# Kernel tuning notes

Measured on AMD Instinct MI355X. Metric: run time of the kernel, lower is better.

## Reference

```python
import jax, jax.numpy as jnp
import numpy as np

HID = 512      # out_channels / HR2O hidden_dim
CIN = 2048     # conv1 input channels (Cf + Cx)
DEPTH = 3
EPS = 1e-5     # GroupNorm eps


def conv2d(x, w, pad):
    return jax.lax.conv_general_dilated(
        x, w, window_strides=(1, 1), padding=[(pad, pad), (pad, pad)],
        dimension_numbers=('NCHW', 'OIHW', 'NCHW'))


def hr2o(x, wq, wk, wv, wm, gamma, beta):
    # x: [N, C, H, W]
    q = conv2d(x, wq, 1)
    k = conv2d(x, wk, 1)
    v = conv2d(x, wv, 1)
    # (query.unsqueeze(1) * key.unsqueeze(0)).sum(2) / sqrt(C) -> [N, N, H, W]
    att = jnp.einsum('qchw,kchw->qkhw', q, k) / jnp.sqrt(jnp.float32(HID))
    att = jax.nn.softmax(att, axis=1)  # softmax over key dim
    # (att.unsqueeze(2) * value).sum(1) -> [N, C, H, W]
    vf = jnp.einsum('qkhw,kchw->qchw', att, v)
    # GroupNorm(1, C): normalize over (C, H, W), per-channel affine
    mu = jnp.mean(vf, axis=(1, 2, 3), keepdims=True)
    var = jnp.var(vf, axis=(1, 2, 3), keepdims=True)
    vf = (vf - mu) * jax.lax.rsqrt(var + EPS)
    vf = vf * gamma[None, :, None, None] + beta[None, :, None, None]
    vf = jax.nn.relu(vf)
    vf = conv2d(vf, wm, 1)
    # Dropout(0.2) is identity in eval mode
    return x + vf


def setup_inputs() -> dict:
    key = jax.random.key(0)
    ks = jax.random.split(key, 12)
    N, B = 32, 8
    Cx, Cf, H, W = 1024, 1024, 16, 16
    s = 0.02
    return {
        'x': jax.random.normal(ks[0], (N, Cx, 4, 7, 7), jnp.float32),
        'feat': jax.random.normal(ks[1], (B, Cf, 1, H, W), jnp.float32),
        'rois': jax.random.randint(ks[2], (N, 5), 0, B, jnp.int32),
        'w1': jax.random.normal(ks[3], (HID, CIN, 1, 1), jnp.float32) * s,
        'w2': jax.random.normal(ks[4], (HID, HID, 3, 3), jnp.float32) * s,
        'wq': jax.random.normal(ks[5], (DEPTH, HID, HID, 3, 3), jnp.float32) * s,
        'wk': jax.random.normal(ks[6], (DEPTH, HID, HID, 3, 3), jnp.float32) * s,
        'wv': jax.random.normal(ks[7], (DEPTH, HID, HID, 3, 3), jnp.float32) * s,
        'wm': jax.random.normal(ks[8], (DEPTH, HID, HID, 3, 3), jnp.float32) * s,
        'gamma': jnp.ones((DEPTH, HID), jnp.float32),
        'beta': jnp.zeros((DEPTH, HID), jnp.float32),
    }


def reference(x, feat, rois, w1, w2, wq, wk, wv, wm, gamma, beta):
    n, cx = x.shape[0], x.shape[1]
    # AdaptiveMaxPool3d(1) -> [N, Cx, 1, 1, 1]
    xp = jnp.max(x, axis=(2, 3, 4), keepdims=True)
    h, w = feat.shape[-2], feat.shape[-1]
    roi_inds = rois[:, 0].astype(jnp.int32)
    roi_gfeat = feat[roi_inds]                              # [N, Cf, 1, H, W]
    x_tile = jnp.broadcast_to(xp, (n, cx, 1, h, w))         # repeat(1,1,1,h,w)
    nf = jnp.concatenate([roi_gfeat, x_tile], axis=1)[:, :, 0]  # squeeze(2)
    nf = jax.nn.relu(conv2d(nf, w1, 0))                     # 1x1 conv
    nf = jax.nn.relu(conv2d(nf, w2, 0))                     # 3x3 conv, no pad
    for i in range(DEPTH):
        nf = hr2o(nf, wq[i], wk[i], wv[i], wm[i], gamma[i], beta[i])
    nf = jnp.mean(nf, axis=(2, 3), keepdims=True)[:, :, None]  # gap -> [N,C,1,1,1]
    return jnp.concatenate([xp, nf], axis=1)                # [N, Cx+HID, 1, 1, 1]
```

## Files before the change

kernel.cpp:

```cpp
#include <hip/hip_runtime.h>


typedef __attribute__((ext_vector_type(8))) short bhalf8;
typedef __attribute__((ext_vector_type(4))) float floatx4;

#define ACT_N 131072
#define W3SZ  2359296

__device__ inline float b2f(unsigned short u) {
  union { unsigned int i; float f; } x; x.i = ((unsigned int)u) << 16; return x.f;
}
__device__ inline unsigned short f2b(float f) {
  union { float f; unsigned int i; } x; x.f = f;
  return (unsigned short)((x.i + 0x7FFFu + ((x.i >> 16) & 1u)) >> 16);
}
__device__ inline void gload_lds16(const unsigned short* g, bhalf8* l) {
  __builtin_amdgcn_global_load_lds(
      (const __attribute__((address_space(1))) unsigned int*)(const void*)g,
      (__attribute__((address_space(3))) unsigned int*)(void*)l, 16, 0, 0);
}
template <int N> __device__ inline void waitvm() {
  asm volatile("s_waitcnt vmcnt(%0)" :: "i"(N) : "memory");
}
__device__ inline void phase_barrier_pre() {
  __builtin_amdgcn_sched_barrier(0);
  __builtin_amdgcn_s_barrier();
  __builtin_amdgcn_sched_barrier(0);
}
__device__ inline void phase_barrier_post() {
  __builtin_amdgcn_sched_barrier(0);
  __builtin_amdgcn_s_barrier();
  __builtin_amdgcn_sched_barrier(0);
}

__global__ void pool_max_kernel(const float* __restrict__ x, float* __restrict__ xp,
                                float* __restrict__ out) {
  int tid = threadIdx.x;
  int wid = blockIdx.x * 4 + (tid >> 6);
  int lane = tid & 63;
  int n = wid >> 10, c = wid & 1023;
  const float* p = x + (size_t)wid * 196;
  float v = -3.4e38f;
  v = fmaxf(v, p[lane]);
  v = fmaxf(v, p[lane + 64]);
  v = fmaxf(v, p[lane + 128]);
  if (lane < 4) v = fmaxf(v, p[lane + 192]);
#pragma unroll
  for (int off = 32; off >= 1; off >>= 1) v = fmaxf(v, __shfl_xor(v, off));
  if (lane == 0) { xp[wid] = v; out[(size_t)n * 1536 + c] = v; }
}

__global__ void bias1_kernel(const float* __restrict__ w1, const float* __restrict__ xp,
                             float* __restrict__ bias1) {
  int tid = threadIdx.x;
  int wid = blockIdx.x * 4 + (tid >> 6);
  int lane = tid & 63;
  int n = wid >> 9, o = wid & 511;
  const float* wr = w1 + (size_t)o * 2048 + 1024;
  const float* xr = xp + (size_t)n * 1024;
  float s = 0.f;
#pragma unroll
  for (int r = 0; r < 16; r++) { int c = lane + r * 64; s += wr[c] * xr[c]; }
#pragma unroll
  for (int off = 32; off >= 1; off >>= 1) s += __shfl_xor(s, off);
  if (lane == 0) bias1[wid] = s;
}

__global__ __launch_bounds__(256) void wprep3_kernel(
    const float* __restrict__ w2, const float* __restrict__ wq,
    const float* __restrict__ wk, const float* __restrict__ wv,
    const float* __restrict__ wm, unsigned short* __restrict__ Wg2) {
  int ks = blockIdx.x, ot = blockIdx.y, tid = blockIdx.z;
  int t = threadIdx.x;
  const float* src;
  if (tid == 0) src = w2;
  else {
    int d = (tid - 1) >> 2, r = (tid - 1) & 3;
    src = (r == 0 ? wq : r == 1 ? wk : r == 2 ? wv : wm) + (size_t)d * W3SZ;
  }
  __shared__ unsigned short S[64 * 288];
  const float* sb = src + (size_t)ot * 64 * 4608 + (size_t)ks * 288;
  for (int j = 0; j < 72; j++) {
    int flat = j * 256 + t;
    int o = flat / 288, ci = flat % 288;
    S[flat] = f2b(sb[(size_t)o * 4608 + ci]);
  }
  __syncthreads();
  unsigned short* dst = Wg2 + (((size_t)(tid * 8 + ot) * 16 + ks) * 2304) * 8;
#pragma unroll
  for (int s = 0; s < 9; s++) {
    int u = t + s * 256;
    int g = u / 768, rem = u % 768;
    int rl = rem >> 6, o = rem & 63;
    int dh = rl >> 2, kg = rl & 3;
    int t9src = dh * 3 + g;
    bhalf8 v;
#pragma unroll
    for (int j = 0; j < 8; j++) v[j] = (short)S[o * 288 + (kg * 8 + j) * 9 + t9src];
    *(bhalf8*)(dst + (size_t)u * 8) = v;
  }
}

__global__ void w1prep_kernel(const float* __restrict__ w1, unsigned short* __restrict__ W1g) {
  int ks = blockIdx.x, ot = blockIdx.y, t = threadIdx.x;
  int kg = t >> 6, o = t & 63;
  const float* s = w1 + (size_t)(ot * 64 + o) * 2048 + ks * 32 + kg * 8;
  bhalf8 v;
#pragma unroll
  for (int j = 0; j < 8; j++) v[j] = (short)f2b(s[j]);
  *(bhalf8*)(W1g + (((size_t)ot * 32 + ks) * 256 + t) * 8) = v;
}

__global__ __launch_bounds__(256) void ftprep_kernel(
    const float* __restrict__ feat, unsigned short* __restrict__ featT) {
  int img = blockIdx.z, c0 = blockIdx.y * 64, p0 = blockIdx.x * 64;
  int t = threadIdx.x;
  int a = t >> 6, b = t & 63;
  __shared__ float S[64][65];
#pragma unroll
  for (int j = 0; j < 16; j++) {
    int r = a * 16 + j;
    S[r][b] = feat[((size_t)img * 1024 + c0 + r) * 256 + p0 + b];
  }
  __syncthreads();
#pragma unroll
  for (int j = 0; j < 16; j++) {
    int pl = a * 16 + j;
    featT[((size_t)img * 256 + p0 + pl) * 1024 + c0 + b] = f2b(S[b][pl]);
  }
}

template <int TAPS, int KTOT, int WAVES, int NREP, int PSPLIT,
          bool RELU, bool ADD, bool BIAS, bool VALID>
__global__ __launch_bounds__(WAVES * 64) void conv_mfma_kernel(
    const unsigned short* __restrict__ Xg, const int* __restrict__ rois,
    const unsigned short* __restrict__ Wg, const float* __restrict__ bias,
    unsigned short* __restrict__ Out) {
  constexpr int THREADS = WAVES * 64;
  constexpr int NK = KTOT / 32;
  static_assert(PSPLIT * WAVES * NREP * 16 == 256, "p coverage");

  int n = blockIdx.y;
  int ot = blockIdx.x / PSPLIT;
  int pq = blockIdx.x % PSPLIT;
  int t = threadIdx.x;
  int wv = t >> 6, l = t & 63, l15 = l & 15, l4 = l >> 4;
  int pbase = (pq * WAVES + wv) * (NREP * 16);
  const unsigned short* xb =
      Xg + (rois ? (size_t)rois[n * 5] * 256 * KTOT : (size_t)n * 256 * KTOT);
  floatx4 acc[4][NREP] = {};

  if constexpr (TAPS == 9) {
    constexpr int LW = 768 / THREADS;
    constexpr int LX = 1024 / THREADS;
    static_assert(768 % THREADS == 0 && 1024 % THREADS == 0, "stage div");
    __shared__ bhalf8 Xs[2][1024];
    __shared__ bhalf8 Wl[3][768];

    auto stageX = [&](int xbuf, int ks) {
#pragma unroll
      for (int i = 0; i < LX; i++) {
        int base = i * THREADS + wv * 64;
        int u = base + l;
        int p = u & 255, kg = u >> 8;
        gload_lds16(xb + (size_t)p * KTOT + ks * 32 + kg * 8, &Xs[xbuf][base]);
      }
    };
    auto stageW = [&](int wbuf, int ks, int g) {
      const unsigned short* wb =
          Wg + (((size_t)ot * NK + ks) * 2304 + g * 768) * 8;
#pragma unroll
      for (int i = 0; i < LW; i++) {
        int base = i * THREADS + wv * 64;
        gload_lds16(wb + (size_t)(base + l) * 8, &Wl[wbuf][base]);
      }
    };
    auto computeG = [&](const bhalf8* X, const bhalf8* W, int g) {
      bhalf8 BW[NREP + 2];
#pragma unroll
      for (int w10 = 0; w10 < NREP + 2; w10++) {
        int row = (pbase + w10 * 16 + l15 + g) & 255;
        BW[w10] = X[l4 * 256 + row];
      }
      bhalf8 A[3][4];
#pragma unroll
      for (int dh = 0; dh < 3; dh++)
#pragma unroll
        for (int of = 0; of < 4; of++)
          A[dh][of] = W[(dh * 4 + l4) * 64 + of * 16 + l15];
      __builtin_amdgcn_s_setprio(1);
#pragma unroll
      for (int dh = 0; dh < 3; dh++)
#pragma unroll
        for (int of = 0; of < 4; of++)
#pragma unroll
          for (int pf = 0; pf < NREP; pf++)
            acc[of][pf] = __builtin_amdgcn_mfma_f32_16x16x32_bf16(
                A[dh][of], BW[pf + dh], acc[of][pf], 0, 0, 0);
      __builtin_amdgcn_s_setprio(0);
    };

    stageW(0, 0, 0); stageX(0, 0);
    stageW(1, 0, 1);

    for (int ks = 0; ks < NK - 1; ks++) {
      const bhalf8* X = Xs[ks & 1];
      stageW(2, ks, 2);
      waitvm<2 * LW>();
      phase_barrier_pre();
      computeG(X, Wl[0], 0);
      phase_barrier_post();
      stageW(0, ks + 1, 0); stageX((ks + 1) & 1, ks + 1);
      waitvm<2 * LW + LX>();
      phase_barrier_pre();
      computeG(X, Wl[1], 1);
      phase_barrier_post();
      stageW(1, ks + 1, 1);
      waitvm<2 * LW + LX>();
      phase_barrier_pre();
      computeG(X, Wl[2], 2);
      phase_barrier_post();
    }
    {
      const bhalf8* X = Xs[(NK - 1) & 1];
      stageW(2, NK - 1, 2);
      waitvm<2 * LW>();
      phase_barrier_pre();
      computeG(X, Wl[0], 0);
      phase_barrier_post();
      waitvm<LW>();
      phase_barrier_pre();
      computeG(X, Wl[1], 1);
      phase_barrier_post();
      waitvm<0>();
      phase_barrier_pre();
      computeG(X, Wl[2], 2);
      phase_barrier_post();
    }
  } else {
    constexpr int LW = 256 / THREADS;
    constexpr int LX = 1024 / THREADS;
    static_assert(256 % THREADS == 0 && 1024 % THREADS == 0, "stage div");
    __shared__ bhalf8 Xs[3][1024];
    __shared__ bhalf8 Wl[3][256];

    auto stage1 = [&](int b, int ks) {
#pragma unroll
      for (int i = 0; i < LX; i++) {
        int base = i * THREADS + wv * 64;
        int u = base + l;
        int p = u & 255, kg = u >> 8;
        gload_lds16(xb + (size_t)p * KTOT + ks * 32 + kg * 8, &Xs[b][base]);
      }
      const unsigned short* wb = Wg + (((size_t)ot * NK + ks) * 256) * 8;
#pragma unroll
      for (int i = 0; i < LW; i++) {
        int base = i * THREADS + wv * 64;
        gload_lds16(wb + (size_t)(base + l) * 8, &Wl[b][base]);
      }
    };
    auto compute1 = [&](const bhalf8* X, const bhalf8* W) {
      bhalf8 B[NREP];
#pragma unroll
      for (int pf = 0; pf < NREP; pf++) {
        int row = (pbase + pf * 16 + l15) & 255;
        B[pf] = X[l4 * 256 + row];
      }
      bhalf8 A[4];
#pragma unroll
      for (int of = 0; of < 4; of++) A[of] = W[l4 * 64 + of * 16 + l15];
      __builtin_amdgcn_s_setprio(1);
#pragma unroll
      for (int of = 0; of < 4; of++)
#pragma unroll
        for (int pf = 0; pf < NREP; pf++)
          acc[of][pf] = __builtin_amdgcn_mfma_f32_16x16x32_bf16(
              A[of], B[pf], acc[of][pf], 0, 0, 0);
      __builtin_amdgcn_s_setprio(0);
    };

    stage1(0, 0);
    stage1(1, 1);
    int b = 0;
    for (int ks = 0; ks < NK - 2; ks++) {
      int b2 = b + 2; if (b2 >= 3) b2 -= 3;
      stage1(b2, ks + 2);
      waitvm<2 * (LW + LX)>();
      phase_barrier_pre();
      compute1(Xs[b], Wl[b]);
      phase_barrier_post();
      b = b + 1; if (b >= 3) b -= 3;
    }
    waitvm<LW + LX>();
    phase_barrier_pre();
    compute1(Xs[b], Wl[b]);
    phase_barrier_post();
    b = b + 1; if (b >= 3) b -= 3;
    waitvm<0>();
    phase_barrier_pre();
    compute1(Xs[b], Wl[b]);
    phase_barrier_post();
  }

#pragma unroll
  for (int of = 0; of < 4; of++) {
    int og = ot * 64 + of * 16 + l4 * 4;
    int tensor = og >> 9, ol = og & 511;
#pragma unroll
    for (int pf = 0; pf < NREP; pf++) {
      int p = pbase + pf * 16 + l15;
      int po = p;
      if (VALID) {
        int h = p >> 4, w = p & 15;
        if (h >= 14 || w >= 14) continue;
        po = (h + 1) * 16 + (w + 1);
      }
      unsigned short* dp = Out + (((size_t)tensor * 32 + n) * 256 + po) * 512 + ol;
      float vv[4];
#pragma unroll
      for (int r2 = 0; r2 < 4; r2++) vv[r2] = acc[of][pf][r2];
      if (BIAS) {
#pragma unroll
        for (int r2 = 0; r2 < 4; r2++) vv[r2] += bias[(size_t)n * 512 + ol + r2];
      }
      if (ADD) {
        ushort4 old = *(const ushort4*)dp;
        vv[0] += b2f(old.x); vv[1] += b2f(old.y); vv[2] += b2f(old.z); vv[3] += b2f(old.w);
      }
      if (RELU) {
#pragma unroll
        for (int r2 = 0; r2 < 4; r2++) vv[r2] = fmaxf(vv[r2], 0.f);
      }
      ushort4 st = { f2b(vv[0]), f2b(vv[1]), f2b(vv[2]), f2b(vv[3]) };
      *(ushort4*)dp = st;
    }
  }
}

__global__ __launch_bounds__(256) void vtrans_kernel(
    const unsigned short* __restrict__ v, unsigned short* __restrict__ vt) {
  int ppc = blockIdx.x;
  int pp = (ppc / 14 + 1) * 16 + ppc % 14 + 1;
  int t = threadIdx.x;
  __shared__ unsigned short S[32 * 512];
#pragma unroll
  for (int i = 0; i < 8; i++) {
    int u = i * 256 + t;
    int kn = u >> 6, c8 = (u & 63) * 8;
    *(bhalf8*)&S[kn * 512 + c8] = *(const bhalf8*)(v + ((size_t)kn * 256 + pp) * 512 + c8);
  }
  __syncthreads();
#pragma unroll
  for (int half = 0; half < 2; half++) {
    int c = half * 256 + t;
    unsigned int col[16];
#pragma unroll
    for (int j = 0; j < 16; j++)
      col[j] = (unsigned int)S[(2 * j) * 512 + c] |
               ((unsigned int)S[(2 * j + 1) * 512 + c] << 16);
    unsigned short* dst = vt + ((size_t)ppc * 512 + c) * 32;
#pragma unroll
    for (int j = 0; j < 4; j++) {
      uint4 P = { col[j * 4], col[j * 4 + 1], col[j * 4 + 2], col[j * 4 + 3] };
      *(uint4*)(dst + j * 8) = P;
    }
  }
}

__global__ __launch_bounds__(64) void attfused_kernel(
    const unsigned short* __restrict__ q, const unsigned short* __restrict__ k,
    const unsigned short* __restrict__ vt, unsigned short* __restrict__ out,
    float* __restrict__ gnpart) {
  int pp = blockIdx.x;
  int h = pp >> 4, w = pp & 15;
  int l = threadIdx.x, l15 = l & 15, l4 = l >> 4;
  if (h < 1 || h > 14 || w < 1 || w > 14) {
    uint4 z = {0u, 0u, 0u, 0u};
#pragma unroll
    for (int qn = 0; qn < 32; qn++)
      *(uint4*)(out + ((size_t)qn * 256 + pp) * 512 + l * 8) = z;
    return;
  }
  int ppc = (h - 1) * 14 + (w - 1);

  floatx4 sc[2][2] = {};
#pragma unroll
  for (int kb = 0; kb < 16; kb++) {
    bhalf8 A[2], B[2];
#pragma unroll
    for (int of = 0; of < 2; of++)
      A[of] = *(const bhalf8*)(k + ((size_t)(of * 16 + l15) * 256 + pp) * 512 + kb * 32 + l4 * 8);
#pragma unroll
    for (int pf = 0; pf < 2; pf++)
      B[pf] = *(const bhalf8*)(q + ((size_t)(pf * 16 + l15) * 256 + pp) * 512 + kb * 32 + l4 * 8);
#pragma unroll
    for (int of = 0; of < 2; of++)
#pragma unroll
      for (int pf = 0; pf < 2; pf++)
        sc[of][pf] = __builtin_amdgcn_mfma_f32_16x16x32_bf16(A[of], B[pf], sc[of][pf], 0, 0, 0);
  }

  __shared__ unsigned short p_lds[32 * 32];
  const float scale = 0.044194173824159216f;
#pragma unroll
  for (int pf = 0; pf < 2; pf++) {
    float v8[8];
    float m = -3.4e38f;
#pragma unroll
    for (int of = 0; of < 2; of++)
#pragma unroll
      for (int r = 0; r < 4; r++) {
        float x = sc[of][pf][r] * scale;
        v8[of * 4 + r] = x;
        m = fmaxf(m, x);
      }
    m = fmaxf(m, __shfl_xor(m, 16));
    m = fmaxf(m, __shfl_xor(m, 32));
    float s = 0.f;
#pragma unroll
    for (int i = 0; i < 8; i++) { v8[i] = __expf(v8[i] - m); s += v8[i]; }
    s += __shfl_xor(s, 16);
    s += __shfl_xor(s, 32);
    float inv = 1.f / s;
#pragma unroll
    for (int of = 0; of < 2; of++) {
      ushort4 pk = { f2b(v8[of * 4 + 0] * inv), f2b(v8[of * 4 + 1] * inv),
                     f2b(v8[of * 4 + 2] * inv), f2b(v8[of * 4 + 3] * inv) };
      *(ushort4*)&p_lds[(pf * 16 + l15) * 32 + of * 16 + l4 * 4] = pk;
    }
  }

  bhalf8 PB[2];
#pragma unroll
  for (int qf = 0; qf < 2; qf++)
    PB[qf] = *(const bhalf8*)&p_lds[(qf * 16 + l15) * 32 + l4 * 8];
  float gs[2] = {0.f, 0.f}, gss[2] = {0.f, 0.f};
  const unsigned short* vtb = vt + (size_t)ppc * 512 * 32;
#pragma unroll
  for (int chunk = 0; chunk < 4; chunk++) {
    bhalf8 VA[8];
#pragma unroll
    for (int co = 0; co < 8; co++)
      VA[co] = *(const bhalf8*)(vtb + (size_t)(chunk * 128 + co * 16 + l15) * 32 + l4 * 8);
#pragma unroll
    for (int co = 0; co < 8; co++)
#pragma unroll
      for (int qf = 0; qf < 2; qf++) {
        floatx4 pa = __builtin_amdgcn_mfma_f32_16x16x32_bf16(
            VA[co], PB[qf], (floatx4){0.f, 0.f, 0.f, 0.f}, 0, 0, 0);
        float x0 = pa[0], x1 = pa[1], x2 = pa[2], x3 = pa[3];
        gs[qf] += x0 + x1 + x2 + x3;
        gss[qf] += x0 * x0 + x1 * x1 + x2 * x2 + x3 * x3;
        ushort4 st = { f2b(x0), f2b(x1), f2b(x2), f2b(x3) };
        int qn = qf * 16 + l15;
        int c = chunk * 128 + co * 16 + l4 * 4;
        *(ushort4*)(out + ((size_t)qn * 256 + pp) * 512 + c) = st;
      }
  }
#pragma unroll
  for (int qf = 0; qf < 2; qf++) {
    gs[qf] += __shfl_xor(gs[qf], 16);  gs[qf] += __shfl_xor(gs[qf], 32);
    gss[qf] += __shfl_xor(gss[qf], 16); gss[qf] += __shfl_xor(gss[qf], 32);
  }
  if (l4 == 0) {
#pragma unroll
    for (int qf = 0; qf < 2; qf++) {
      int qn = qf * 16 + l15;
      gnpart[((size_t)ppc * 32 + qn) * 2]     = gs[qf];
      gnpart[((size_t)ppc * 32 + qn) * 2 + 1] = gss[qf];
    }
  }
}

__global__ __launch_bounds__(256) void gnapply3_kernel(
    unsigned short* __restrict__ x, const float* __restrict__ gnpart,
    const float* __restrict__ gamma, const float* __restrict__ beta) {
  int n = blockIdx.y, half = blockIdx.x, t = threadIdx.x;
  float s = 0.f, ss = 0.f;
  if (t < 196) {
    s  = gnpart[((size_t)t * 32 + n) * 2];
    ss = gnpart[((size_t)t * 32 + n) * 2 + 1];
  }
#pragma unroll
  for (int off = 32; off >= 1; off >>= 1) { s += __shfl_xor(s, off); ss += __shfl_xor(ss, off); }
  __shared__ float sm[8];
  int wv = t >> 6, ln = t & 63;
  if (ln == 0) { sm[wv] = s; sm[4 + wv] = ss; }
  __syncthreads();
  float S = sm[0] + sm[1] + sm[2] + sm[3];
  float SS = sm[4] + sm[5] + sm[6] + sm[7];
  const float M = 512.f * 196.f;
  float mu = S / M;
  float var = SS / M - mu * mu;
  float inv = rsqrtf(var + 1e-5f);
  int c2 = t * 2;
  unsigned short* xb = x + (size_t)n * ACT_N;
  float g0 = gamma[c2], g1 = gamma[c2 + 1];
  float be0 = beta[c2], be1 = beta[c2 + 1];
  for (int i = 0; i < 98; i++) {
    int ppc = half * 98 + i;
    int pp = (ppc / 14 + 1) * 16 + ppc % 14 + 1;
    unsigned int vv = *(unsigned int*)(xb + pp * 512 + c2);
    float a = (b2f((unsigned short)vv) - mu) * inv * g0 + be0;
    float b = (b2f((unsigned short)(vv >> 16)) - mu) * inv * g1 + be1;
    a = fmaxf(a, 0.f); b = fmaxf(b, 0.f);
    *(unsigned int*)(xb + pp * 512 + c2) =
        (unsigned int)f2b(a) | ((unsigned int)f2b(b) << 16);
  }
}

__global__ void fmean2_kernel(const unsigned short* __restrict__ x, float* __restrict__ out) {
  int n = blockIdx.x, t = threadIdx.x;
  const unsigned short* xb = x + (size_t)n * ACT_N;
  float s0 = 0.f, s1 = 0.f;
  for (int i = 0; i < 196; i++) {
    int pp = (i / 14 + 1) * 16 + (i % 14) + 1;
    unsigned int vv = *(const unsigned int*)(xb + pp * 512 + t * 2);
    s0 += b2f((unsigned short)vv);
    s1 += b2f((unsigned short)(vv >> 16));
  }
  out[(size_t)n * 1536 + 1024 + t * 2]     = s0 * (1.f / 196.f);
  out[(size_t)n * 1536 + 1024 + t * 2 + 1] = s1 * (1.f / 196.f);
}

extern "C" void kernel_launch(void* const* d_in, const int* in_sizes, int n_in,
                              void* d_out, int out_size, void* d_ws, size_t ws_size,
                              hipStream_t stream) {
  const float* x     = (const float*)d_in[0];
  const float* feat  = (const float*)d_in[1];
  const int*   rois  = (const int*)d_in[2];
  const float* w1    = (const float*)d_in[3];
  const float* w2    = (const float*)d_in[4];
  const float* wq    = (const float*)d_in[5];
  const float* wk    = (const float*)d_in[6];
  const float* wv    = (const float*)d_in[7];
  const float* wm    = (const float*)d_in[8];
  const float* gamma = (const float*)d_in[9];
  const float* beta  = (const float*)d_in[10];
  float* out = (float*)d_out;

  float* wsf   = (float*)d_ws;
  float* xp    = wsf;
  float* bias1 = xp + 32768;
  float* stats = bias1 + 16384;
  float* attf  = stats + 64;
  unsigned short* ub    = (unsigned short*)(attf + 262144);
  unsigned short* featT = ub;
  unsigned short* W1g   = featT + 2097152;
  unsigned short* Wg2   = W1g + 524288;
  unsigned short* bufq  = Wg2 + 30670848;
  unsigned short* bufk  = bufq + 4194304;
  unsigned short* bufv  = bufk + 4194304;
  unsigned short* bufx  = bufv + 4194304;
  unsigned short* vt    = (unsigned short*)d_ws;
  float* gnpart = (float*)(bufx + 4194304);

  hipMemsetAsync(bufx, 0, (size_t)4194304 * 2, stream);

  pool_max_kernel<<<8192, 256, 0, stream>>>(x, xp, out);
  bias1_kernel<<<4096, 256, 0, stream>>>(w1, xp, bias1);
  wprep3_kernel<<<dim3(16, 8, 13), 256, 0, stream>>>(w2, wq, wk, wv, wm, Wg2);
  w1prep_kernel<<<dim3(32, 8), 256, 0, stream>>>(w1, W1g);
  ftprep_kernel<<<dim3(4, 16, 8), 256, 0, stream>>>(feat, featT);

  conv_mfma_kernel<1, 1024, 4, 4, 1, true, false, true, false>
      <<<dim3(8, 32), 256, 0, stream>>>(featT, rois, W1g, bias1, bufq);
  conv_mfma_kernel<9, 512, 4, 4, 1, true, false, false, true>
      <<<dim3(8, 32), 256, 0, stream>>>(bufq, nullptr, Wg2, nullptr, bufx);

  for (int d = 0; d < 3; d++) {
    conv_mfma_kernel<9, 512, 4, 4, 1, false, false, false, true>
        <<<dim3(24, 32), 256, 0, stream>>>(bufx, nullptr,
            Wg2 + (size_t)(1 + 4 * d) * W3SZ, nullptr, bufq);
    vtrans_kernel<<<196, 256, 0, stream>>>(bufv, vt);
    attfused_kernel<<<256, 64, 0, stream>>>(bufq, bufk, vt, bufq, gnpart);
    gnapply3_kernel<<<dim3(2, 32), 256, 0, stream>>>(bufq, gnpart,
        gamma + d * 512, beta + d * 512);
    conv_mfma_kernel<9, 512, 4, 4, 1, false, true, false, true>
        <<<dim3(8, 32), 256, 0, stream>>>(bufq, nullptr,
            Wg2 + (size_t)(4 + 4 * d) * W3SZ, nullptr, bufx);
  }

  fmean2_kernel<<<32, 256, 0, stream>>>(bufx, out);
}
```

Before: 788.4 us.

## Load conv weights straight into registers and cut per-phase barriers

Weight tiles are no longer staged through LDS. Each wave now loads its MFMA A-fragments directly from global memory into double-buffered register arrays, and only the activation tile goes through LDS with two buffers. The schedule is rewritten so one barrier per k-step replaces the two barriers around every tap-group compute, with vmcnt waits sized to the register prefetches. The aim is to remove LDS traffic and barrier stalls, at the cost of extra register pressure and weight fragments being read redundantly from global or L2 by every block that shares them.

Result: slower. 889.2 us (+12.8%).

```diff
diff --git a/kernel.cpp b/kernel.cpp
--- a/kernel.cpp
+++ b/kernel.cpp
@@ -22,16 +22,7 @@
 template <int N> __device__ inline void waitvm() {
   asm volatile("s_waitcnt vmcnt(%0)" :: "i"(N) : "memory");
 }
-__device__ inline void phase_barrier_pre() {
-  __builtin_amdgcn_sched_barrier(0);
-  __builtin_amdgcn_s_barrier();
-  __builtin_amdgcn_sched_barrier(0);
-}
-__device__ inline void phase_barrier_post() {
-  __builtin_amdgcn_sched_barrier(0);
-  __builtin_amdgcn_s_barrier();
-  __builtin_amdgcn_sched_barrier(0);
-}
+__device__ inline void SB() { __builtin_amdgcn_sched_barrier(0); }
 
 __global__ void pool_max_kernel(const float* __restrict__ x, float* __restrict__ xp,
                                 float* __restrict__ out) {
@@ -138,7 +129,10 @@
     unsigned short* __restrict__ Out) {
   constexpr int THREADS = WAVES * 64;
   constexpr int NK = KTOT / 32;
+  constexpr int LX = 1024 / THREADS;
   static_assert(PSPLIT * WAVES * NREP * 16 == 256, "p coverage");
+  static_assert(1024 % THREADS == 0, "stage div");
+  __shared__ bhalf8 Xs[2][1024];
 
   int n = blockIdx.y;
   int ot = blockIdx.x / PSPLIT;
@@ -150,44 +144,32 @@
       Xg + (rois ? (size_t)rois[n * 5] * 256 * KTOT : (size_t)n * 256 * KTOT);
   floatx4 acc[4][NREP] = {};
 
+  auto stageX = [&](int xbuf, int ks) {
+#pragma unroll
+    for (int i = 0; i < LX; i++) {
+      int base = i * THREADS + wv * 64;
+      int u = base + l;
+      int p = u & 255, kg = u >> 8;
+      gload_lds16(xb + (size_t)p * KTOT + ks * 32 + kg * 8, &Xs[xbuf][base]);
+    }
+  };
+
   if constexpr (TAPS == 9) {
-    constexpr int LW = 768 / THREADS;
-    constexpr int LX = 1024 / THREADS;
-    static_assert(768 % THREADS == 0 && 1024 % THREADS == 0, "stage div");
-    __shared__ bhalf8 Xs[2][1024];
-    __shared__ bhalf8 Wl[3][768];
-
-    auto stageX = [&](int xbuf, int ks) {
-#pragma unroll
-      for (int i = 0; i < LX; i++) {
-        int base = i * THREADS + wv * 64;
-        int u = base + l;
-        int p = u & 255, kg = u >> 8;
-        gload_lds16(xb + (size_t)p * KTOT + ks * 32 + kg * 8, &Xs[xbuf][base]);
-      }
+    const unsigned short* wB = Wg + (size_t)ot * NK * 2304 * 8;
+    bhalf8 A0[12], A1[12];
+    auto issueA = [&](bhalf8 (&dst)[12], int ks, int g) {
+      const unsigned short* wp = wB + ((size_t)ks * 2304 + g * 768 + l4 * 64 + l15) * 8;
+#pragma unroll
+      for (int dh = 0; dh < 3; dh++)
+#pragma unroll
+        for (int of = 0; of < 4; of++)
+          dst[dh * 4 + of] = *(const bhalf8*)(wp + (size_t)(dh * 256 + of * 16) * 8);
     };
-    auto stageW = [&](int wbuf, int ks, int g) {
-      const unsigned short* wb =
-          Wg + (((size_t)ot * NK + ks) * 2304 + g * 768) * 8;
-#pragma unroll
-      for (int i = 0; i < LW; i++) {
-        int base = i * THREADS + wv * 64;
-        gload_lds16(wb + (size_t)(base + l) * 8, &Wl[wbuf][base]);
-      }
-    };
-    auto computeG = [&](const bhalf8* X, const bhalf8* W, int g) {
+    auto computeG = [&](const bhalf8* X, const bhalf8 (&A)[12], int g) {
       bhalf8 BW[NREP + 2];
 #pragma unroll
-      for (int w10 = 0; w10 < NREP + 2; w10++) {
-        int row = (pbase + w10 * 16 + l15 + g) & 255;
-        BW[w10] = X[l4 * 256 + row];
-      }
-      bhalf8 A[3][4];
-#pragma unroll
-      for (int dh = 0; dh < 3; dh++)
-#pragma unroll
-        for (int of = 0; of < 4; of++)
-          A[dh][of] = W[(dh * 4 + l4) * 64 + of * 16 + l15];
+      for (int w10 = 0; w10 < NREP + 2; w10++)
+        BW[w10] = X[l4 * 256 + ((pbase + w10 * 16 + l15 + g) & 255)];
       __builtin_amdgcn_s_setprio(1);
 #pragma unroll
       for (int dh = 0; dh < 3; dh++)
@@ -196,79 +178,67 @@
 #pragma unroll
           for (int pf = 0; pf < NREP; pf++)
             acc[of][pf] = __builtin_amdgcn_mfma_f32_16x16x32_bf16(
-                A[dh][of], BW[pf + dh], acc[of][pf], 0, 0, 0);
+                A[dh * 4 + of], BW[pf + dh], acc[of][pf], 0, 0, 0);
       __builtin_amdgcn_s_setprio(0);
     };
 
-    stageW(0, 0, 0); stageX(0, 0);
-    stageW(1, 0, 1);
-
-    for (int ks = 0; ks < NK - 1; ks++) {
-      const bhalf8* X = Xs[ks & 1];
-      stageW(2, ks, 2);
-      waitvm<2 * LW>();
-      phase_barrier_pre();
-      computeG(X, Wl[0], 0);
-      phase_barrier_post();
-      stageW(0, ks + 1, 0); stageX((ks + 1) & 1, ks + 1);
-      waitvm<2 * LW + LX>();
-      phase_barrier_pre();
-      computeG(X, Wl[1], 1);
-      phase_barrier_post();
-      stageW(1, ks + 1, 1);
-      waitvm<2 * LW + LX>();
-      phase_barrier_pre();
-      computeG(X, Wl[2], 2);
-      phase_barrier_post();
+    stageX(0, 0);
+    issueA(A0, 0, 0); SB();
+    waitvm<12>();
+    __builtin_amdgcn_s_barrier(); SB();
+
+    for (int ks = 0; ks < NK - 2; ks += 2) {
+      const bhalf8* Xe = Xs[ks & 1];
+      issueA(A1, ks, 1); SB();
+      waitvm<12>(); computeG(Xe, A0, 0); SB();
+      issueA(A0, ks, 2); stageX((ks + 1) & 1, ks + 1); SB();
+      waitvm<16>(); computeG(Xe, A1, 1); SB();
+      issueA(A1, ks + 1, 0); SB();
+      waitvm<16>(); computeG(Xe, A0, 2); SB();
+      waitvm<12>();
+      __builtin_amdgcn_s_barrier(); SB();
+      const bhalf8* Xo = Xs[(ks + 1) & 1];
+      issueA(A0, ks + 1, 1); SB();
+      waitvm<12>(); computeG(Xo, A1, 0); SB();
+      issueA(A1, ks + 1, 2); stageX(ks & 1, ks + 2); SB();
+      waitvm<16>(); computeG(Xo, A0, 1); SB();
+      issueA(A0, ks + 2, 0); SB();
+      waitvm<16>(); computeG(Xo, A1, 2); SB();
+      waitvm<12>();
+      __builtin_amdgcn_s_barrier(); SB();
     }
     {
-      const bhalf8* X = Xs[(NK - 1) & 1];
-      stageW(2, NK - 1, 2);
-      waitvm<2 * LW>();
-      phase_barrier_pre();
-      computeG(X, Wl[0], 0);
-      phase_barrier_post();
-      waitvm<LW>();
-      phase_barrier_pre();
-      computeG(X, Wl[1], 1);
-      phase_barrier_post();
-      waitvm<0>();
-      phase_barrier_pre();
-      computeG(X, Wl[2], 2);
-      phase_barrier_post();
+      const int ks = NK - 2;
+      const bhalf8* Xe = Xs[ks & 1];
+      issueA(A1, ks, 1); SB();
+      waitvm<12>(); computeG(Xe, A0, 0); SB();
+      issueA(A0, ks, 2); stageX((ks + 1) & 1, ks + 1); SB();
+      waitvm<16>(); computeG(Xe, A1, 1); SB();
+      issueA(A1, ks + 1, 0); SB();
+      waitvm<16>(); computeG(Xe, A0, 2); SB();
+      waitvm<12>();
+      __builtin_amdgcn_s_barrier(); SB();
+      const bhalf8* Xo = Xs[(ks + 1) & 1];
+      issueA(A0, ks + 1, 1); SB();
+      waitvm<12>(); computeG(Xo, A1, 0); SB();
+      issueA(A1, ks + 1, 2); SB();
+      waitvm<12>(); computeG(Xo, A0, 1); SB();
+      waitvm<0>(); computeG(Xo, A1, 2); SB();
     }
   } else {
-    constexpr int LW = 256 / THREADS;
-    constexpr int LX = 1024 / THREADS;
-    static_assert(256 % THREADS == 0 && 1024 % THREADS == 0, "stage div");
-    __shared__ bhalf8 Xs[3][1024];
-    __shared__ bhalf8 Wl[3][256];
-
-    auto stage1 = [&](int b, int ks) {
-#pragma unroll
-      for (int i = 0; i < LX; i++) {
-        int base = i * THREADS + wv * 64;
-        int u = base + l;
-        int p = u & 255, kg = u >> 8;
-        gload_lds16(xb + (size_t)p * KTOT + ks * 32 + kg * 8, &Xs[b][base]);
-      }
-      const unsigned short* wb = Wg + (((size_t)ot * NK + ks) * 256) * 8;
-#pragma unroll
-      for (int i = 0; i < LW; i++) {
-        int base = i * THREADS + wv * 64;
-        gload_lds16(wb + (size_t)(base + l) * 8, &Wl[b][base]);
-      }
+    const unsigned short* wB = Wg + (size_t)ot * NK * 256 * 8;
+    bhalf8 A0[4], A1[4];
+    auto issueA1 = [&](bhalf8 (&dst)[4], int ks) {
+      const unsigned short* wp = wB + ((size_t)ks * 256 + l4 * 64 + l15) * 8;
+#pragma unroll
+      for (int of = 0; of < 4; of++)
+        dst[of] = *(const bhalf8*)(wp + (size_t)(of * 16) * 8);
     };
-    auto compute1 = [&](const bhalf8* X, const bhalf8* W) {
+    auto compute1 = [&](const bhalf8* X, const bhalf8 (&A)[4]) {
       bhalf8 B[NREP];
 #pragma unroll
-      for (int pf = 0; pf < NREP; pf++) {
-        int row = (pbase + pf * 16 + l15) & 255;
-        B[pf] = X[l4 * 256 + row];
-      }
-      bhalf8 A[4];
-#pragma unroll
-      for (int of = 0; of < 4; of++) A[of] = W[l4 * 64 + of * 16 + l15];
+      for (int pf = 0; pf < NREP; pf++)
+        B[pf] = X[l4 * 256 + ((pbase + pf * 16 + l15) & 255)];
       __builtin_amdgcn_s_setprio(1);
 #pragma unroll
       for (int of = 0; of < 4; of++)
@@ -279,27 +249,25 @@
       __builtin_amdgcn_s_setprio(0);
     };
 
-    stage1(0, 0);
-    stage1(1, 1);
-    int b = 0;
-    for (int ks = 0; ks < NK - 2; ks++) {
-      int b2 = b + 2; if (b2 >= 3) b2 -= 3;
-      stage1(b2, ks + 2);
-      waitvm<2 * (LW + LX)>();
-      phase_barrier_pre();
-      compute1(Xs[b], Wl[b]);
-      phase_barrier_post();
-      b = b + 1; if (b >= 3) b -= 3;
-    }
-    waitvm<LW + LX>();
-    phase_barrier_pre();
-    compute1(Xs[b], Wl[b]);
-    phase_barrier_post();
-    b = b + 1; if (b >= 3) b -= 3;
-    waitvm<0>();
-    phase_barrier_pre();
-    compute1(Xs[b], Wl[b]);
-    phase_barrier_post();
+    stageX(0, 0);
+    issueA1(A0, 0); SB();
+    waitvm<4>();
+    __builtin_amdgcn_s_barrier(); SB();
+    for (int ks = 0; ks < NK - 2; ks += 2) {
+      stageX((ks + 1) & 1, ks + 1); issueA1(A1, ks + 1); SB();
+      waitvm<8>(); compute1(Xs[ks & 1], A0); SB();
+      waitvm<4>(); __builtin_amdgcn_s_barrier(); SB();
+      stageX(ks & 1, ks + 2); issueA1(A0, ks + 2); SB();
+      waitvm<8>(); compute1(Xs[(ks + 1) & 1], A1); SB();
+      waitvm<4>(); __builtin_amdgcn_s_barrier(); SB();
+    }
+    {
+      const int ks = NK - 2;
+      stageX((ks + 1) & 1, ks + 1); issueA1(A1, ks + 1); SB();
+      waitvm<8>(); compute1(Xs[ks & 1], A0); SB();
+      waitvm<4>(); __builtin_amdgcn_s_barrier(); SB();
+      waitvm<0>(); compute1(Xs[(ks + 1) & 1], A1); SB();
+    }
   }
 
 #pragma unroll
```
